# Optimization experiments

Hardware: AMD Instinct MI355X
Metric: run time of the kernel (lower is better)

Reference implementation:

```python
import jax, jax.numpy as jnp
import numpy as np
import math

B, H, N, L = 8, 512, 64, 2048


def setup_inputs() -> dict:
    key = jax.random.key(0)
    k_u, k_c, k_dt, k_d, k_w, k_b, k_ar, k_ai = jax.random.split(key, 8)
    u = jax.random.normal(k_u, (B, H, L), dtype=jnp.float32)
    # C ~ complex randn, stored as (..., 2) real/imag pairs (torch.view_as_real)
    C_ri = jax.random.normal(k_c, (H, N, 2), dtype=jnp.float32)
    # log_dt ~ Uniform(log(dt_min), log(dt_max))
    lo, hi = math.log(0.001), math.log(0.1)
    log_dt = jax.random.uniform(k_dt, (H,), dtype=jnp.float32) * (hi - lo) + lo
    D = jax.random.normal(k_d, (H,), dtype=jnp.float32)
    # Conv1d(H, 2H, kernel_size=1) -> weight (2H, H), bias (2H), kaiming-ish scale
    W = jax.random.normal(k_w, (2 * H, H), dtype=jnp.float32) / math.sqrt(H)
    b = jax.random.normal(k_b, (2 * H,), dtype=jnp.float32) * 0.01
    # Fixed diagonal state matrix A: Re(A) uniform in [-0.9, -0.8), Im(A) random
    a_re = -0.9 + 0.1 * jax.random.uniform(k_ar, (N,), dtype=jnp.float32)
    a_im = math.pi * jnp.arange(N, dtype=jnp.float32)  # stable oscillation freqs
    A_ri = jnp.stack([a_re, a_im], axis=-1)
    return {"u": u, "C_ri": C_ri, "log_dt": log_dt, "D": D, "W": W, "b": b, "A_ri": A_ri}


def _forward(u, C_ri, log_dt, D, W, b, A_ri):
    Lseq = u.shape[-1]
    C = C_ri[..., 0] + 1j * C_ri[..., 1]          # (H, N) complex
    A = A_ri[..., 0] + 1j * A_ri[..., 1]          # (N,) complex
    dt = jnp.exp(log_dt)                           # (H,)
    dtA = dt[:, None] * A[None, :]                 # (H, N)
    # Vandermonde: exp(dtA * l) for l in [0, L)  -> (H, N, L) complex
    K = jnp.exp(dtA[:, :, None] * jnp.arange(Lseq, dtype=jnp.float32))
    Ct = C * (jnp.exp(dtA) - 1.0) / A              # (H, N)
    k = 2.0 * jnp.einsum('hn,hnl->hl', Ct, K).real  # (H, L) real kernel
    # FFT long convolution (linear conv via length-2L circular conv)
    nfft = 2 * Lseq
    y = jnp.fft.irfft(jnp.fft.rfft(u, n=nfft) * jnp.fft.rfft(k, n=nfft), n=nfft)[..., :Lseq]
    y = y + D[:, None] * u                         # skip connection
    y = jax.nn.gelu(y, approximate=False)          # torch nn.GELU default = exact erf
    # Conv1d kernel_size=1 == per-position linear, then GLU over channel dim
    z = jnp.einsum('oh,bhl->bol', W, y) + b[:, None]  # (B, 2H, L)
    a, g = jnp.split(z, 2, axis=-2)
    return a * jax.nn.sigmoid(g)                   # (B, H, L)


def reference(u, C_ri, log_dt, D, W, b, A_ri):
    return _forward(u, C_ri, log_dt, D, W, b, A_ri)
```

## Files before the change

kernel.cpp:

```cpp
#include <hip/hip_runtime.h>
#include <math.h>

#define Hh 512
#define Nn 64
#define Ll 2048
#define Bb 8

typedef float f32x4 __attribute__((ext_vector_type(4)));
typedef __bf16 bf16x8 __attribute__((ext_vector_type(8)));

__device__ __forceinline__ unsigned short f2b(float x) {
  unsigned u = __builtin_bit_cast(unsigned, x);
  u += 0x7FFFu + ((u >> 16) & 1u);
  return (unsigned short)(u >> 16);
}
__device__ __forceinline__ float b2f(unsigned short b) {
  unsigned u = ((unsigned)b) << 16;
  return __builtin_bit_cast(float, u);
}

union BF8 {
  unsigned short us[8];
  bf16x8 v;
  uint4 q;
};

__device__ __forceinline__ uint4 cvt8q(const float* p) {
  float4 a = *(const float4*)p;
  float4 b = *(const float4*)(p + 4);
  BF8 o;
  o.us[0] = f2b(a.x); o.us[1] = f2b(a.y); o.us[2] = f2b(a.z); o.us[3] = f2b(a.w);
  o.us[4] = f2b(b.x); o.us[5] = f2b(b.y); o.us[6] = f2b(b.z); o.us[7] = f2b(b.w);
  return o.q;
}

__device__ __forceinline__ float gelu_f(float y) {
  float t = y * y;
  float p = y * fmaf(0.0713548162726f, t, 1.59576912161f);
  float e = __expf(-p);
  return y / (1.0f + e);
}

__global__ __launch_bounds__(512) void prep_kernel(
    const float* __restrict__ C_ri, const float* __restrict__ log_dt,
    const float* __restrict__ A_ri, const float* __restrict__ W,
    unsigned short* __restrict__ A1, unsigned short* __restrict__ A2,
    float* __restrict__ lamQ, unsigned short* __restrict__ Wimg) {
  int tid = threadIdx.x;
  if (blockIdx.x >= 512) {
    int id = (blockIdx.x - 512) * 512 + tid;
    int slot = id & 3, row = (id >> 2) & 127, kt = (id >> 9) & 15, ot = id >> 13;
    int o = (row < 64) ? (ot * 64 + row) : (512 + ot * 64 + row - 64);
    uint4 v = cvt8q(W + (size_t)o * 512 + kt * 32 + slot * 8);
    int sp = slot ^ ((row >> 1) & 3);
    *(uint4*)((char*)Wimg + (((size_t)ot * 16 + kt) * 8192) + row * 64 + sp * 16) = v;
    return;
  }
  __shared__ char sm[49152];
  __shared__ float kqs[64];
  __shared__ float kpart[8][64];
  float* kt = (float*)sm;
  char* A1s = sm;
  char* A2s = sm + 16384;
  int h = blockIdx.x;
  int n = tid & 63, part = tid >> 6;

  float dt = expf(log_dt[h]);
  float ar = A_ri[2 * n], ai = A_ri[2 * n + 1];
  float er = expf(dt * ar);
  float sn, cs;
  sincosf(dt * ai, &sn, &cs);
  float lr = er * cs, li = er * sn;
  float em1r = lr - 1.0f, em1i = li;
  float cr = C_ri[(h * 64 + n) * 2], ci = C_ri[(h * 64 + n) * 2 + 1];
  float numr = cr * em1r - ci * em1i;
  float numi = cr * em1i + ci * em1r;
  float den = ar * ar + ai * ai;
  float ctr = (numr * ar + numi * ai) / den;
  float cti = (numi * ar - numr * ai) / den;
  float l8r = lr, l8i = li;
#pragma unroll
  for (int s = 0; s < 3; ++s) {
    float t = l8r * l8r - l8i * l8i;
    l8i = 2.0f * l8r * l8i;
    l8r = t;
  }
  if (part == 0) {
    float qr = l8r, qi = l8i;
#pragma unroll
    for (int s = 0; s < 3; ++s) {
      float t = qr * qr - qi * qi;
      qi = 2.0f * qr * qi;
      qr = t;
    }
    lamQ[h * 128 + 2 * n] = qr;
    lamQ[h * 128 + 2 * n + 1] = qi;
  }
  float lpr = 1.0f, lpi = 0.0f;
  for (int s = 0; s < part; ++s) {
    float t = lpr * l8r - lpi * l8i;
    lpi = lpr * l8i + lpi * l8r;
    lpr = t;
  }
  int e0 = part * 8;
  {
    float vr = ctr * lpr - cti * lpi, vi = ctr * lpi + cti * lpr;
#pragma unroll
    for (int j = 0; j < 8; ++j) {
      kt[(e0 + j) * 64 + n] = vr;
      float t = vr * lr - vi * li;
      vi = vr * li + vi * lr;
      vr = t;
    }
  }
  __syncthreads();
  {
    float s = 0.0f;
#pragma unroll
    for (int j = 0; j < 8; ++j) s += kt[n * 64 + ((e0 + j + n) & 63)];
    kpart[part][n] = s;
  }
  __syncthreads();
  if (part == 0) {
    float s = 0.0f;
#pragma unroll
    for (int p2 = 0; p2 < 8; ++p2) s += kpart[p2][n];
    kqs[n] = 2.0f * s;
  }
  __syncthreads();
  {
    BF8 R0, I0;
    float vr = lpr, vi = lpi;
#pragma unroll
    for (int j = 0; j < 8; ++j) {
      int idx = 7 - j;
      R0.us[idx] = f2b(vr);
      I0.us[idx] = f2b(vi);
      float t = vr * lr - vi * li;
      vi = vr * li + vi * lr;
      vr = t;
    }
    int qlo = 56 - e0;
    int rowR = 2 * n, rowI = 2 * n + 1;
    *(uint4*)(A1s + ((rowR * 128 + 2 * qlo) ^ ((rowR & 7) << 4))) = R0.q;
    *(uint4*)(A1s + ((rowI * 128 + 2 * qlo) ^ ((rowI & 7) << 4))) = I0.q;
  }
  {
    float c1r = ctr * lr - cti * li, c1i = ctr * li + cti * lr;
    float wr = 2.0f * (c1r * lpr - c1i * lpi);
    float wi = 2.0f * (c1r * lpi + c1i * lpr);
#pragma unroll
    for (int j = 0; j < 8; ++j) {
      int t = e0 + j;
      *(unsigned*)(A2s + ((t * 512 + 128 + 4 * n) ^ ((t & 7) << 4))) =
          (unsigned)f2b(wr) | ((unsigned)f2b(-wi) << 16);
      float tm = wr * lr - wi * li;
      wi = wr * li + wi * lr;
      wr = tm;
    }
  }
  {
    int tau = n;
    BF8 o;
#pragma unroll
    for (int j = 0; j < 8; ++j) {
      int q = e0 + j;
      o.us[j] = (q <= tau) ? f2b(kqs[tau - q]) : (unsigned short)0;
    }
    *(uint4*)(A2s + ((tau * 512 + 2 * e0) ^ ((tau & 7) << 4))) = o.q;
  }
  __syncthreads();
#pragma unroll
  for (int i = 0; i < 2; ++i) {
    int byte = (i * 512 + tid) * 16;
    int row = byte >> 7;
    *(uint4*)((char*)A1 + (size_t)h * 16384 + byte) =
        *(const uint4*)(A1s + (byte ^ ((row & 7) << 4)));
  }
#pragma unroll
  for (int i = 0; i < 4; ++i) {
    int idx = i * 512 + tid;
    int row = idx >> 5;
    int byte = row * 512 + (idx & 31) * 16;
    *(uint4*)((char*)A2 + (size_t)h * 32768 + byte) =
        *(const uint4*)(A2s + (byte ^ ((row & 7) << 4)));
  }
}

__global__ __launch_bounds__(256, 5) void fused_conv_kernel(
    const float* __restrict__ u, const unsigned short* __restrict__ A1,
    const unsigned short* __restrict__ A2, const float* __restrict__ lamQ,
    const float* __restrict__ Dv, unsigned short* __restrict__ gy) {
  __shared__ char SXb[16384];
  __shared__ char Ub[8192];
  __shared__ float2 sX16[2][64];
  int h = blockIdx.x;
  int bs = blockIdx.y * 2;
  int tid = threadIdx.x;
  int w = tid >> 6, lane = tid & 63, lg = lane >> 4, l15 = lane & 15;

  {
    int row = tid >> 2, k0 = (tid & 3) * 16;
    int b = bs + (row >> 5), c = row & 31;
    const float* up = u + ((size_t)(b * Hh + h)) * Ll + c * 64 + k0;
    uint4 v0 = cvt8q(up), v1 = cvt8q(up + 8);
    int base = row * 128 + k0 * 2;
    int swz = (row & 7) << 4;
    *(uint4*)(Ub + (base ^ swz)) = v0;
    *(uint4*)(Ub + ((base + 16) ^ swz)) = v1;
  }
  bf16x8 a1f[2][2];
#pragma unroll
  for (int i = 0; i < 2; ++i) {
    int row = (2 * w + i) * 16 + l15;
#pragma unroll
    for (int kb = 0; kb < 2; ++kb)
      a1f[i][kb] = *(const bf16x8*)(A1 + ((size_t)h * 128 + row) * 64 + kb * 32 + lg * 8);
  }
  __syncthreads();

#pragma unroll
  for (int ct = 0; ct < 4; ++ct) {
    int bc = ct * 16 + l15;
    bf16x8 bu[2];
#pragma unroll
    for (int kb = 0; kb < 2; ++kb)
      bu[kb] = *(const bf16x8*)(Ub + ((bc * 128 + kb * 64 + lg * 16) ^ ((bc & 7) << 4)));
#pragma unroll
    for (int i = 0; i < 2; ++i) {
      f32x4 acc = {0.f, 0.f, 0.f, 0.f};
      acc = __builtin_amdgcn_mfma_f32_16x16x32_bf16(a1f[i][0], bu[0], acc, 0, 0, 0);
      acc = __builtin_amdgcn_mfma_f32_16x16x32_bf16(a1f[i][1], bu[1], acc, 0, 0, 0);
      int n2q = (2 * w + i) * 16 + lg * 4;
      uint2 pk;
      pk.x = f2b(acc[0]) | ((unsigned)f2b(acc[1]) << 16);
      pk.y = f2b(acc[2]) | ((unsigned)f2b(acc[3]) << 16);
      *(uint2*)(SXb + ((bc * 256 + n2q * 2) ^ ((bc & 7) << 4))) = pk;
    }
  }
  __syncthreads();

  bf16x8 a2f[6];
  int rowA = w * 16 + l15;
#pragma unroll
  for (int kb = 0; kb < 6; ++kb)
    a2f[kb] = *(const bf16x8*)(A2 + ((size_t)h * 64 + rowA) * 256 + kb * 32 + lg * 8);

  int nn = tid & 63, bpart = tid >> 6;
  int rbloc = bpart >> 1, rhalf = bpart & 1;
  float lqr = lamQ[h * 128 + 2 * nn], lqi = lamQ[h * 128 + 2 * nn + 1];
  {
    float Xr = 0.f, Xi = 0.f;
    int cbase = rbloc * 32 + rhalf * 16;
    for (int c = 0; c < 16; ++c) {
      int bc = cbase + c;
      int byte = (bc * 256 + 4 * nn) ^ ((bc & 7) << 4);
      unsigned ps = *(const unsigned*)(SXb + byte);
      *(unsigned*)(SXb + byte) = (unsigned)f2b(Xr) | ((unsigned)f2b(Xi) << 16);
      float Sr = b2f((unsigned short)(ps & 0xFFFF));
      float Si = b2f((unsigned short)(ps >> 16));
      float nXr = lqr * Xr - lqi * Xi + Sr;
      float nXi = lqr * Xi + lqi * Xr + Si;
      Xr = nXr;
      Xi = nXi;
    }
    if (rhalf == 0) sX16[rbloc][nn] = make_float2(Xr, Xi);
  }
  __syncthreads();
  if (rhalf) {
    float2 x16 = sX16[rbloc][nn];
    float cr = x16.x, ci = x16.y;
    int cbase = rbloc * 32 + 16;
#pragma unroll
    for (int c = 0; c < 16; ++c) {
      int bc = cbase + c;
      int byte = (bc * 256 + 4 * nn) ^ ((bc & 7) << 4);
      unsigned pv = *(const unsigned*)(SXb + byte);
      float vr = b2f((unsigned short)(pv & 0xFFFF)) + cr;
      float vi = b2f((unsigned short)(pv >> 16)) + ci;
      *(unsigned*)(SXb + byte) = (unsigned)f2b(vr) | ((unsigned)f2b(vi) << 16);
      float t = cr * lqr - ci * lqi;
      ci = cr * lqi + ci * lqr;
      cr = t;
    }
  }
  __syncthreads();

  float Dh = Dv[h];
  int t0 = w * 16 + lg * 4;
  f32x4 acc4[4];
  uint2 usk[4];
#pragma unroll
  for (int ct = 0; ct < 4; ++ct) {
    int bc = ct * 16 + l15;
    f32x4 acc = {0.f, 0.f, 0.f, 0.f};
#pragma unroll
    for (int kb = 0; kb < 2; ++kb) {
      bf16x8 bu = *(const bf16x8*)(Ub + ((bc * 128 + kb * 64 + lg * 16) ^ ((bc & 7) << 4)));
      acc = __builtin_amdgcn_mfma_f32_16x16x32_bf16(a2f[kb], bu, acc, 0, 0, 0);
    }
#pragma unroll
    for (int kb = 2; kb < 6; ++kb) {
      bf16x8 bx = *(const bf16x8*)(SXb + ((bc * 256 + ((kb - 2) * 32 + lg * 8) * 2) ^ ((bc & 7) << 4)));
      acc = __builtin_amdgcn_mfma_f32_16x16x32_bf16(a2f[kb], bx, acc, 0, 0, 0);
    }
    acc4[ct] = acc;
    usk[ct] = *(const uint2*)(Ub + ((bc * 128 + t0 * 2) ^ ((bc & 7) << 4)));
  }
  __syncthreads();

#pragma unroll
  for (int ct = 0; ct < 4; ++ct) {
    int bc = ct * 16 + l15;
    const unsigned short* up = (const unsigned short*)&usk[ct];
    unsigned short e[4];
#pragma unroll
    for (int r = 0; r < 4; ++r) {
      float y = fmaf(Dh, b2f(up[r]), acc4[ct][r]);
      e[r] = f2b(gelu_f(y));
    }
    uint2 pk;
    pk.x = e[0] | ((unsigned)e[1] << 16);
    pk.y = e[2] | ((unsigned)e[3] << 16);
    *(uint2*)(Ub + ((bc * 128 + t0 * 2) ^ ((bc & 7) << 4))) = pk;
  }
  __syncthreads();

#pragma unroll
  for (int i = 0; i < 2; ++i) {
    int j = tid + 256 * i;
    int row = j >> 3, q = j & 7;
    int byte = row * 128 + q * 16;
    uint4 v = *(const uint4*)(Ub + (byte ^ ((row & 7) << 4)));
    int b = bs + (row >> 5), c = row & 31;
    *(uint4*)(gy + ((size_t)(b * Hh + h)) * Ll + c * 64 + q * 8) = v;
  }
}

__global__ __launch_bounds__(512, 4) void glu_kernel(
    const unsigned short* __restrict__ Wimg, const unsigned short* __restrict__ gy,
    const float* __restrict__ bias, float* __restrict__ out) {
  __shared__ char sA[2][2][8192];
  __shared__ char sB[2][8192];
  int lt = blockIdx.x;
  int oz = blockIdx.y;
  int b = lt >> 4, lseg = lt & 15;
  int t = threadIdx.x;
  int lane = t & 63, lg = lane >> 4, l15 = lane & 15;
  int w = t >> 6;
  int otl = w & 1;
  int ot = oz * 2 + otl;
  int wm = (w >> 2) & 1, wn = (w >> 1) & 1;
  int doB = (t < 256);
  int p = (t >> 4) & 15, cg = t & 15;
  const char* Abase0 = (const char*)Wimg + (size_t)(oz * 2) * 131072;
  const char* Abase1 = (const char*)Wimg + (size_t)(oz * 2 + 1) * 131072;
  const unsigned short* gybase = gy + (size_t)b * Hh * Ll + lseg * 128 + cg * 8 + 2 * p * Ll;

  int offA[2], offG[2];
#pragma unroll
  for (int mt = 0; mt < 2; ++mt) {
    int rA = wm * 32 + mt * 16 + l15;
    offA[mt] = rA * 64 + ((lg ^ ((rA >> 1) & 3)) << 4);
    int rG = rA + 64;
    offG[mt] = rG * 64 + ((lg ^ ((rG >> 1) & 3)) << 4);
  }
  int offB[4];
#pragma unroll
  for (int nt = 0; nt < 4; ++nt) {
    int rB = wn * 64 + nt * 16 + l15;
    int pr = ((rB >> 3) << 3) | ((rB & 7) ^ ((rB >> 3) & 7));
    offB[nt] = (lg << 11) + (pr << 4);
  }
  int offW[8];
#pragma unroll
  for (int j = 0; j < 8; ++j) {
    int pr = (cg << 3) | (j ^ (cg & 7));
    offW[j] = ((p >> 2) << 11) + (pr << 4) + ((p & 3) << 2);
  }

  f32x4 accA[2][4], accG[2][4];
#pragma unroll
  for (int mt = 0; mt < 2; ++mt)
#pragma unroll
    for (int nt = 0; nt < 4; ++nt) {
      accA[mt][nt] = (f32x4){0.f, 0.f, 0.f, 0.f};
      accG[mt][nt] = (f32x4){0.f, 0.f, 0.f, 0.f};
    }

  {
    __builtin_amdgcn_global_load_lds(Abase0 + t * 16, (char*)&sA[0][0][0] + t * 16, 16, 0, 0);
    __builtin_amdgcn_global_load_lds(Abase1 + t * 16, (char*)&sA[0][1][0] + t * 16, 16, 0, 0);
    if (doB) {
      BF8 r0, r1;
      r0.q = *(const uint4*)gybase;
      r1.q = *(const uint4*)(gybase + Ll);
#pragma unroll
      for (int j = 0; j < 8; ++j)
        *(unsigned*)(&sB[0][0] + offW[j]) =
            (unsigned)r0.us[j] | ((unsigned)r1.us[j] << 16);
    }
  }
  __syncthreads();

  for (int kt = 0; kt < 16; ++kt) {
    int cur = kt & 1;
    BF8 r0, r1;
    if (kt < 15) {
      __builtin_amdgcn_global_load_lds(Abase0 + (kt + 1) * 8192 + t * 16,
                                       (char*)&sA[cur ^ 1][0][0] + t * 16, 16, 0, 0);
      __builtin_amdgcn_global_load_lds(Abase1 + (kt + 1) * 8192 + t * 16,
                                       (char*)&sA[cur ^ 1][1][0] + t * 16, 16, 0, 0);
      if (doB) {
        r0.q = *(const uint4*)(gybase + (size_t)(kt + 1) * 32 * Ll);
        r1.q = *(const uint4*)(gybase + (size_t)(kt + 1) * 32 * Ll + Ll);
      }
    }
    const char* bufA = &sA[cur][otl][0];
    const char* bufB = &sB[cur][0];
    bf16x8 aA[2], aG[2], bB[4];
#pragma unroll
    for (int mt = 0; mt < 2; ++mt) {
      aA[mt] = *(const bf16x8*)(bufA + offA[mt]);
      aG[mt] = *(const bf16x8*)(bufA + offG[mt]);
    }
#pragma unroll
    for (int nt = 0; nt < 4; ++nt)
      bB[nt] = *(const bf16x8*)(bufB + offB[nt]);
#pragma unroll
    for (int mt = 0; mt < 2; ++mt)
#pragma unroll
      for (int nt = 0; nt < 4; ++nt) {
        accA[mt][nt] = __builtin_amdgcn_mfma_f32_16x16x32_bf16(bB[nt], aA[mt], accA[mt][nt], 0, 0, 0);
        accG[mt][nt] = __builtin_amdgcn_mfma_f32_16x16x32_bf16(bB[nt], aG[mt], accG[mt][nt], 0, 0, 0);
      }
    if (kt < 15 && doB) {
      char* db = &sB[cur ^ 1][0];
#pragma unroll
      for (int j = 0; j < 8; ++j)
        *(unsigned*)(db + offW[j]) =
            (unsigned)r0.us[j] | ((unsigned)r1.us[j] << 16);
    }
    __syncthreads();
  }

#pragma unroll
  for (int mt = 0; mt < 2; ++mt) {
    int oA = ot * 64 + wm * 32 + mt * 16 + l15;
    float ba = bias[oA];
    float bg = bias[512 + oA];
    float* orow = out + ((size_t)(b * Hh) + oA) * Ll + lseg * 128 + wn * 64 + lg * 4;
#pragma unroll
    for (int nt = 0; nt < 4; ++nt) {
      float4 res;
      float* rp = (float*)&res;
#pragma unroll
      for (int r = 0; r < 4; ++r) {
        float a = accA[mt][nt][r] + ba;
        float g = accG[mt][nt][r] + bg;
        rp[r] = a * (1.0f / (1.0f + __expf(-g)));
      }
      *(float4*)(orow + nt * 16) = res;
    }
  }
}

extern "C" void kernel_launch(void* const* d_in, const int* in_sizes, int n_in,
                              void* d_out, int out_size, void* d_ws,
                              size_t ws_size, hipStream_t stream) {
  const float* u      = (const float*)d_in[0];
  const float* C_ri   = (const float*)d_in[1];
  const float* log_dt = (const float*)d_in[2];
  const float* Dv     = (const float*)d_in[3];
  const float* W      = (const float*)d_in[4];
  const float* bias   = (const float*)d_in[5];
  const float* A_ri   = (const float*)d_in[6];
  float* out = (float*)d_out;

  char* ws = (char*)d_ws;
  unsigned short* A1   = (unsigned short*)ws;
  unsigned short* A2   = (unsigned short*)(ws + 8388608);
  float*          lamQ = (float*)(ws + 25165824);
  unsigned short* Wimg = (unsigned short*)(ws + 25427968);
  unsigned short* gy   = (unsigned short*)(ws + 26476544);

  prep_kernel<<<640, 512, 0, stream>>>(C_ri, log_dt, A_ri, W, A1, A2, lamQ, Wimg);
  fused_conv_kernel<<<dim3(Hh, 4), 256, 0, stream>>>(u, A1, A2, lamQ, Dv, gy);
  glu_kernel<<<dim3(128, 4), 512, 0, stream>>>(Wimg, gy, bias, out);
}
```

Before: 59.73 us.

## Triple-buffer weight tiles in GLU GEMM with partial vmcnt waits

Moves the weight (A) tiles in the GLU GEMM kernel from double to triple buffering in LDS, prefetching two k-steps ahead with global_load_lds. The full __syncthreads is replaced by an explicit s_waitcnt vmcnt(2) plus s_barrier, so the newest A prefetch can stay in flight across the barrier. This aims to hide global-load latency better. In exchange it adds 16KB of LDS per block, which may lower occupancy, and it depends on the vmcnt counting being exact.

```diff
diff --git a/kernel.cpp b/kernel.cpp
--- a/kernel.cpp
+++ b/kernel.cpp
@@ -340,7 +340,7 @@
 __global__ __launch_bounds__(512, 4) void glu_kernel(
     const unsigned short* __restrict__ Wimg, const unsigned short* __restrict__ gy,
     const float* __restrict__ bias, float* __restrict__ out) {
-  __shared__ char sA[2][2][8192];
+  __shared__ char sA[3][2][8192];
   __shared__ char sB[2][8192];
   int lt = blockIdx.x;
   int oz = blockIdx.y;
@@ -356,14 +356,16 @@
   const char* Abase0 = (const char*)Wimg + (size_t)(oz * 2) * 131072;
   const char* Abase1 = (const char*)Wimg + (size_t)(oz * 2 + 1) * 131072;
   const unsigned short* gybase = gy + (size_t)b * Hh * Ll + lseg * 128 + cg * 8 + 2 * p * Ll;
+  char* sAb = &sA[0][0][0];
+  char* sBb = &sB[0][0];
 
   int offA[2], offG[2];
 #pragma unroll
   for (int mt = 0; mt < 2; ++mt) {
     int rA = wm * 32 + mt * 16 + l15;
-    offA[mt] = rA * 64 + ((lg ^ ((rA >> 1) & 3)) << 4);
+    offA[mt] = otl * 8192 + rA * 64 + ((lg ^ ((rA >> 1) & 3)) << 4);
     int rG = rA + 64;
-    offG[mt] = rG * 64 + ((lg ^ ((rG >> 1) & 3)) << 4);
+    offG[mt] = otl * 8192 + rG * 64 + ((lg ^ ((rG >> 1) & 3)) << 4);
   }
   int offB[4];
 #pragma unroll
@@ -389,35 +391,41 @@
     }
 
   {
-    __builtin_amdgcn_global_load_lds(Abase0 + t * 16, (char*)&sA[0][0][0] + t * 16, 16, 0, 0);
-    __builtin_amdgcn_global_load_lds(Abase1 + t * 16, (char*)&sA[0][1][0] + t * 16, 16, 0, 0);
+    BF8 r0, r1;
     if (doB) {
-      BF8 r0, r1;
       r0.q = *(const uint4*)gybase;
       r1.q = *(const uint4*)(gybase + Ll);
+    }
+    __builtin_amdgcn_global_load_lds(Abase0 + t * 16, sAb + t * 16, 16, 0, 0);
+    __builtin_amdgcn_global_load_lds(Abase1 + t * 16, sAb + 8192 + t * 16, 16, 0, 0);
+    __builtin_amdgcn_global_load_lds(Abase0 + 8192 + t * 16, sAb + 16384 + t * 16, 16, 0, 0);
+    __builtin_amdgcn_global_load_lds(Abase1 + 8192 + t * 16, sAb + 24576 + t * 16, 16, 0, 0);
+    if (doB) {
 #pragma unroll
       for (int j = 0; j < 8; ++j)
-        *(unsigned*)(&sB[0][0] + offW[j]) =
+        *(unsigned*)(sBb + offW[j]) =
             (unsigned)r0.us[j] | ((unsigned)r1.us[j] << 16);
     }
   }
-  __syncthreads();
-
+  asm volatile("s_waitcnt vmcnt(2) lgkmcnt(0)" ::: "memory");
+  __builtin_amdgcn_sched_barrier(0);
+  __builtin_amdgcn_s_barrier();
+  __builtin_amdgcn_sched_barrier(0);
+
+  int cur3 = 0, islot = 2;
   for (int kt = 0; kt < 16; ++kt) {
-    int cur = kt & 1;
     BF8 r0, r1;
-    if (kt < 15) {
-      __builtin_amdgcn_global_load_lds(Abase0 + (kt + 1) * 8192 + t * 16,
-                                       (char*)&sA[cur ^ 1][0][0] + t * 16, 16, 0, 0);
-      __builtin_amdgcn_global_load_lds(Abase1 + (kt + 1) * 8192 + t * 16,
-                                       (char*)&sA[cur ^ 1][1][0] + t * 16, 16, 0, 0);
-      if (doB) {
-        r0.q = *(const uint4*)(gybase + (size_t)(kt + 1) * 32 * Ll);
-        r1.q = *(const uint4*)(gybase + (size_t)(kt + 1) * 32 * Ll + Ll);
-      }
-    }
-    const char* bufA = &sA[cur][otl][0];
-    const char* bufB = &sB[cur][0];
+    if (doB && kt < 15) {
+      r0.q = *(const uint4*)(gybase + (size_t)(kt + 1) * 32 * Ll);
+      r1.q = *(const uint4*)(gybase + (size_t)(kt + 1) * 32 * Ll + Ll);
+    }
+    if (kt < 14) {
+      char* da = sAb + islot * 16384 + t * 16;
+      __builtin_amdgcn_global_load_lds(Abase0 + (kt + 2) * 8192 + t * 16, da, 16, 0, 0);
+      __builtin_amdgcn_global_load_lds(Abase1 + (kt + 2) * 8192 + t * 16, da + 8192, 16, 0, 0);
+    }
+    const char* bufA = sAb + cur3 * 16384;
+    const char* bufB = sBb + (kt & 1) * 8192;
     bf16x8 aA[2], aG[2], bB[4];
 #pragma unroll
     for (int mt = 0; mt < 2; ++mt) {
@@ -434,14 +442,26 @@
         accA[mt][nt] = __builtin_amdgcn_mfma_f32_16x16x32_bf16(bB[nt], aA[mt], accA[mt][nt], 0, 0, 0);
         accG[mt][nt] = __builtin_amdgcn_mfma_f32_16x16x32_bf16(bB[nt], aG[mt], accG[mt][nt], 0, 0, 0);
       }
-    if (kt < 15 && doB) {
-      char* db = &sB[cur ^ 1][0];
+    if (doB && kt < 15) {
+      char* db = sBb + ((kt + 1) & 1) * 8192;
 #pragma unroll
       for (int j = 0; j < 8; ++j)
         *(unsigned*)(db + offW[j]) =
             (unsigned)r0.us[j] | ((unsigned)r1.us[j] << 16);
     }
-    __syncthreads();
+    if (kt < 14) {
+      asm volatile("s_waitcnt vmcnt(2) lgkmcnt(0)" ::: "memory");
+      __builtin_amdgcn_sched_barrier(0);
+      __builtin_amdgcn_s_barrier();
+      __builtin_amdgcn_sched_barrier(0);
+    } else if (kt == 14) {
+      asm volatile("s_waitcnt vmcnt(0) lgkmcnt(0)" ::: "memory");
+      __builtin_amdgcn_sched_barrier(0);
+      __builtin_amdgcn_s_barrier();
+      __builtin_amdgcn_sched_barrier(0);
+    }
+    cur3 = (cur3 == 2) ? 0 : cur3 + 1;
+    islot = (islot == 2) ? 0 : islot + 1;
   }
 
 #pragma unroll
```

Result: slower. 61.17 us (+2.4%).
